# Kernel optimization log

Measured on AMD Instinct MI355X. Metric: run time of the kernel, lower is better.

The kernel has to match this reference:

```python
import jax, jax.numpy as jnp
import numpy as np

H, W = 8, 8
N = 1 + H * W          # 65 tokens (cls + patches)
DIM = 128
HEADS = 8
DH = 32
INNER = HEADS * DH     # 256
B = 64
EPS = 1e-5


def setup_inputs() -> dict:
    key = jax.random.key(0)
    ks = jax.random.split(key, 7)
    x = jax.random.normal(ks[0], (B, N, DIM), dtype=jnp.float32)
    gamma = jnp.ones((DIM,), jnp.float32)
    beta = jnp.zeros((DIM,), jnp.float32)
    # kaiming_uniform-ish init scale for linear weights
    s_qk = float(np.sqrt(1.0 / DIM))
    Wqk = jax.random.uniform(ks[1], (DIM, 2 * INNER), jnp.float32, -s_qk, s_qk)
    # per-(query, key)-position value weights: [n, n, dim, inner]
    Wv = jax.random.uniform(ks[2], (N, N, DIM, INNER), jnp.float32, -s_qk, s_qk)
    s_o = float(np.sqrt(1.0 / INNER))
    Wout = jax.random.uniform(ks[3], (INNER, DIM), jnp.float32, -s_o, s_o)
    bout = jax.random.uniform(ks[4], (DIM,), jnp.float32, -s_o, s_o)
    return {"x": x, "gamma": gamma, "beta": beta, "Wqk": Wqk, "Wv": Wv,
            "Wout": Wout, "bout": bout}


def reference(x, gamma, beta, Wqk, Wv, Wout, bout):
    b, n, d = x.shape
    # LayerNorm
    mu = jnp.mean(x, axis=-1, keepdims=True)
    var = jnp.mean(jnp.square(x - mu), axis=-1, keepdims=True)
    xn = (x - mu) / jnp.sqrt(var + EPS) * gamma + beta
    # q, k projections
    qk = xn @ Wqk                               # [b, n, 2*inner]
    q, k = jnp.split(qk, 2, axis=-1)
    q = q.reshape(b, n, HEADS, DH).transpose(0, 2, 1, 3)  # [b, h, n, dh]
    k = k.reshape(b, n, HEADS, DH).transpose(0, 2, 1, 3)
    scale = DH ** -0.5
    dots = jnp.einsum('bhnd,bhmd->bhnm', q, k) * scale
    attn = jax.nn.softmax(dots, axis=-1)        # [b, h, n, m]
    # per-(n,m) value: v[b,n,m] = xn[b,n] @ Wv[n,m]  -> [b, n, m, inner]
    v = jnp.einsum('bnd,nmde->bnme', xn, Wv)
    v = v.reshape(b, n, n, HEADS, DH)           # [b, n, m, h, dh]
    # weighted sum over keys m
    out = jnp.einsum('bhnm,bnmhd->bnhd', attn, v).reshape(b, n, INNER)
    return out @ Wout + bout
```

## Files before the change

### kernel.cpp

```cpp
#include <hip/hip_runtime.h>

#define EPS 1e-5f

typedef __attribute__((ext_vector_type(8))) short short8;
typedef __attribute__((ext_vector_type(4))) float float4v;

__device__ __forceinline__ unsigned short f2bf(float x) {
  unsigned int u = __builtin_bit_cast(unsigned int, x);
  u += 0x7fffu + ((u >> 16) & 1u);
  return (unsigned short)(u >> 16);
}
__device__ __forceinline__ float bf2f(unsigned short h) {
  unsigned int u = ((unsigned int)h) << 16;
  return __builtin_bit_cast(float, u);
}

__global__ __launch_bounds__(256) void ln_kernel(
    const float* __restrict__ x, const float* __restrict__ gamma,
    const float* __restrict__ beta, float* __restrict__ xn) {
  const int row = blockIdx.x * 4 + (threadIdx.x >> 6);
  const int lane = threadIdx.x & 63;
  const float2 v = ((const float2*)(x + (size_t)row * 128))[lane];
  float s = v.x + v.y;
#pragma unroll
  for (int off = 1; off < 64; off <<= 1) s += __shfl_xor(s, off);
  const float mu = s * (1.f / 128.f);
  const float dx = v.x - mu, dy = v.y - mu;
  float qv = dx * dx + dy * dy;
#pragma unroll
  for (int off = 1; off < 64; off <<= 1) qv += __shfl_xor(qv, off);
  const float rstd = 1.f / sqrtf(qv * (1.f / 128.f) + EPS);
  const float2 g = ((const float2*)gamma)[lane];
  const float2 be = ((const float2*)beta)[lane];
  float2 o;
  o.x = dx * rstd * g.x + be.x;
  o.y = dy * rstd * g.y + be.y;
  ((float2*)(xn + (size_t)row * 128))[lane] = o;
}

__global__ __launch_bounds__(256) void qk_kernel(
    const float* __restrict__ xn, const float* __restrict__ Wqk,
    float* __restrict__ qk) {
  __shared__ float xsx[32][130];
  __shared__ float wsx[128][68];
  const int t = threadIdx.x;
  const int r0 = blockIdx.x * 32, c0 = blockIdx.y * 64;
  for (int i = t; i < 32 * 32; i += 256) {
    int r = i >> 5, c = (i & 31) << 2;
    float4 v = *(const float4*)(xn + (size_t)(r0 + r) * 128 + c);
    float* dst = &xsx[r][c];
    dst[0] = v.x; dst[1] = v.y; dst[2] = v.z; dst[3] = v.w;
  }
  for (int i = t; i < 128 * 16; i += 256) {
    int k = i >> 4, c = (i & 15) << 2;
    *(float4*)&wsx[k][c] = *(const float4*)(Wqk + (size_t)k * 512 + c0 + c);
  }
  __syncthreads();
  const int rr = (t >> 4) * 2, cc = (t & 15) * 4;
  float acc[2][4] = {{0.f, 0.f, 0.f, 0.f}, {0.f, 0.f, 0.f, 0.f}};
  for (int k = 0; k < 128; k++) {
    float4 wv4 = *(const float4*)&wsx[k][cc];
    float x0 = xsx[rr][k], x1 = xsx[rr + 1][k];
    acc[0][0] += x0 * wv4.x; acc[0][1] += x0 * wv4.y;
    acc[0][2] += x0 * wv4.z; acc[0][3] += x0 * wv4.w;
    acc[1][0] += x1 * wv4.x; acc[1][1] += x1 * wv4.y;
    acc[1][2] += x1 * wv4.z; acc[1][3] += x1 * wv4.w;
  }
#pragma unroll
  for (int r = 0; r < 2; r++) {
    float4 o;
    o.x = acc[r][0]; o.y = acc[r][1]; o.z = acc[r][2]; o.w = acc[r][3];
    *(float4*)(qk + (size_t)(r0 + rr + r) * 512 + c0 + cc) = o;
  }
}

__global__ __launch_bounds__(256) void softmax_kernel(
    const float* __restrict__ qk, float* __restrict__ attnT) {
  const int b = blockIdx.x >> 3, h = blockIdx.x & 7;
  __shared__ float qs[65][33];
  __shared__ float ks[65][33];
  __shared__ float dotsS[65][66];
  __shared__ float rsum[65];
  const int t = threadIdx.x;
  for (int i = t; i < 65 * 32; i += 256) {
    int n = i >> 5, d = i & 31;
    size_t base = ((size_t)b * 65 + n) * 512 + h * 32 + d;
    qs[n][d] = qk[base];
    ks[n][d] = qk[base + 256];
  }
  __syncthreads();
  const float scale = 0.17677669529663687f;
  for (int i = t; i < 65 * 65; i += 256) {
    int n = i / 65, mm = i - n * 65;
    float s = 0.f;
#pragma unroll
    for (int d = 0; d < 32; d++) s += qs[n][d] * ks[mm][d];
    dotsS[n][mm] = s * scale;
  }
  __syncthreads();
  if (t < 65) {
    float mx = -1e30f;
    for (int mm = 0; mm < 65; mm++) mx = fmaxf(mx, dotsS[t][mm]);
    float sum = 0.f;
    for (int mm = 0; mm < 65; mm++) {
      float e = __expf(dotsS[t][mm] - mx);
      dotsS[t][mm] = e;
      sum += e;
    }
    rsum[t] = 1.f / sum;
  }
  __syncthreads();
  for (int i = t; i < 65 * 65; i += 256) {
    int n = i / 65, mm = i - n * 65;
    attnT[(((size_t)h * 65 + n) * 65 + mm) * 64 + b] = dotsS[n][mm] * rsum[n];
  }
}

__global__ __launch_bounds__(256, 4) void attnv_kernel(
    const float* __restrict__ xn, const float* __restrict__ attnT,
    const float* __restrict__ Wv, float* __restrict__ innerp) {
  __shared__ __align__(16) unsigned short wvb[2][4096];
  __shared__ float attnL[33 * 64];

  const int nq = blockIdx.x >> 4;
  const int h = (blockIdx.x >> 1) & 7;
  const int half = blockIdx.x & 1;
  const int m0 = half * 33;
  const int mlen = half ? 32 : 33;

  const int t = threadIdx.x, lane = t & 63, w = t >> 6;
  const int boff = w * 16;
  const int er = lane & 15, q = lane >> 4;

  const int e = t & 31;
  const int d0 = (t >> 5) * 16;
  const int kc0 = d0 >> 3;
  const float* wbase = Wv + ((size_t)nq * 65 + m0) * 32768 + (size_t)h * 32 + e;

  float stg[16];
  {
    const float* p = wbase + (size_t)d0 * 256;
#pragma unroll
    for (int i = 0; i < 16; i++) stg[i] = p[(size_t)i * 256];
  }

  {
    const float* abase = attnT + (((size_t)h * 65 + nq) * 65 + m0) * 64;
    for (int i = t; i < mlen * 64; i += 256) attnL[i] = abase[i];
  }

  short8 ah[4], al[4];
  {
    const float* arow = xn + ((size_t)(boff + er) * 65 + nq) * 128;
#pragma unroll
    for (int s = 0; s < 4; s++) {
      float4 v0 = *(const float4*)(arow + s * 32 + q * 8);
      float4 v1 = *(const float4*)(arow + s * 32 + q * 8 + 4);
      float xv[8] = {v0.x, v0.y, v0.z, v0.w, v1.x, v1.y, v1.z, v1.w};
#pragma unroll
      for (int j = 0; j < 8; j++) {
        unsigned short hi = f2bf(xv[j]);
        ah[s][j] = (short)hi;
        al[s][j] = (short)f2bf(xv[j] - bf2f(hi));
      }
    }
  }

  {
    short8 w0, w1;
#pragma unroll
    for (int j = 0; j < 8; j++) {
      w0[j] = (short)f2bf(stg[j]);
      w1[j] = (short)f2bf(stg[8 + j]);
    }
    *(short8*)&wvb[0][e * 128 + ((kc0 ^ (e & 15)) << 3)] = w0;
    *(short8*)&wvb[0][e * 128 + (((kc0 + 1) ^ (e & 15)) << 3)] = w1;
  }
  __syncthreads();

  float4v acc0 = {0.f, 0.f, 0.f, 0.f}, acc1 = {0.f, 0.f, 0.f, 0.f};

  for (int m = 0; m < mlen; m++) {
    const int cur = m & 1;
    if (m + 1 < mlen) {
      const float* p = wbase + (size_t)(m + 1) * 32768 + (size_t)d0 * 256;
#pragma unroll
      for (int i = 0; i < 16; i++) stg[i] = p[(size_t)i * 256];
    }
    const unsigned short* wb = wvb[cur];
    float4v P0 = {0.f, 0.f, 0.f, 0.f}, P1 = {0.f, 0.f, 0.f, 0.f};
#pragma unroll
    for (int s = 0; s < 4; s++) {
      const int kc = 4 * s + q;
      short8 b0 = *(const short8*)&wb[er * 128 + ((kc ^ er) << 3)];
      short8 b1 = *(const short8*)&wb[(er + 16) * 128 + ((kc ^ er) << 3)];
      P0 = __builtin_amdgcn_mfma_f32_16x16x32_bf16(ah[s], b0, P0, 0, 0, 0);
      P1 = __builtin_amdgcn_mfma_f32_16x16x32_bf16(ah[s], b1, P1, 0, 0, 0);
      P0 = __builtin_amdgcn_mfma_f32_16x16x32_bf16(al[s], b0, P0, 0, 0, 0);
      P1 = __builtin_amdgcn_mfma_f32_16x16x32_bf16(al[s], b1, P1, 0, 0, 0);
    }
    {
      const float* ap = attnL + m * 64 + boff + q * 4;
#pragma unroll
      for (int r = 0; r < 4; r++) {
        float av = ap[r];
        acc0[r] += av * P0[r];
        acc1[r] += av * P1[r];
      }
    }
    if (m + 1 < mlen) {
      short8 w0, w1;
#pragma unroll
      for (int j = 0; j < 8; j++) {
        w0[j] = (short)f2bf(stg[j]);
        w1[j] = (short)f2bf(stg[8 + j]);
      }
      unsigned short* wbw = wvb[1 - cur];
      *(short8*)&wbw[e * 128 + ((kc0 ^ (e & 15)) << 3)] = w0;
      *(short8*)&wbw[e * 128 + (((kc0 + 1) ^ (e & 15)) << 3)] = w1;
    }
    __syncthreads();
  }

  float* ip = innerp + (size_t)half * 1064960;
#pragma unroll
  for (int r = 0; r < 4; r++) {
    int b = boff + q * 4 + r;
    size_t o = ((size_t)b * 65 + nq) * 256 + h * 32;
    ip[o + er] = acc0[r];
    ip[o + 16 + er] = acc1[r];
  }
}

__global__ __launch_bounds__(256) void outproj_kernel(
    const float* __restrict__ inner0, const float* __restrict__ inner1,
    const float* __restrict__ Wout, const float* __restrict__ bout,
    float* __restrict__ out) {
  __shared__ float isx[16][258];
  __shared__ float wsx[64][132];
  const int t = threadIdx.x;
  const int r0 = blockIdx.x * 16;
  for (int i = t; i < 16 * 64; i += 256) {
    int r = i >> 6, c = (i & 63) << 2;
    size_t off = (size_t)(r0 + r) * 256 + c;
    float4 v0 = *(const float4*)(inner0 + off);
    float4 v1 = *(const float4*)(inner1 + off);
    float* dst = &isx[r][c];
    dst[0] = v0.x + v1.x; dst[1] = v0.y + v1.y;
    dst[2] = v0.z + v1.z; dst[3] = v0.w + v1.w;
  }
  const int rr = (t >> 5) * 2, cc = (t & 31) * 4;
  float acc[2][4] = {{0.f, 0.f, 0.f, 0.f}, {0.f, 0.f, 0.f, 0.f}};
  for (int kc = 0; kc < 4; kc++) {
    __syncthreads();
    for (int i = t; i < 64 * 32; i += 256) {
      int k = i >> 5, c = (i & 31) << 2;
      *(float4*)&wsx[k][c] = *(const float4*)(Wout + (size_t)(kc * 64 + k) * 128 + c);
    }
    __syncthreads();
#pragma unroll 8
    for (int k = 0; k < 64; k++) {
      float4 wv4 = *(const float4*)&wsx[k][cc];
      float x0 = isx[rr][kc * 64 + k];
      float x1 = isx[rr + 1][kc * 64 + k];
      acc[0][0] += x0 * wv4.x; acc[0][1] += x0 * wv4.y;
      acc[0][2] += x0 * wv4.z; acc[0][3] += x0 * wv4.w;
      acc[1][0] += x1 * wv4.x; acc[1][1] += x1 * wv4.y;
      acc[1][2] += x1 * wv4.z; acc[1][3] += x1 * wv4.w;
    }
  }
  float4 bb = *(const float4*)(bout + cc);
#pragma unroll
  for (int r = 0; r < 2; r++) {
    float4 o;
    o.x = acc[r][0] + bb.x; o.y = acc[r][1] + bb.y;
    o.z = acc[r][2] + bb.z; o.w = acc[r][3] + bb.w;
    *(float4*)(out + (size_t)(r0 + rr + r) * 128 + cc) = o;
  }
}

extern "C" void kernel_launch(void* const* d_in, const int* in_sizes, int n_in,
                              void* d_out, int out_size, void* d_ws, size_t ws_size,
                              hipStream_t stream) {
  const float* x     = (const float*)d_in[0];
  const float* gamma = (const float*)d_in[1];
  const float* beta  = (const float*)d_in[2];
  const float* Wqk   = (const float*)d_in[3];
  const float* Wv    = (const float*)d_in[4];
  const float* Wout  = (const float*)d_in[5];
  const float* bout  = (const float*)d_in[6];
  float* out = (float*)d_out;
  float* ws  = (float*)d_ws;

  float* xn    = ws;
  float* qk    = ws + 532480;
  float* attnT = ws + 2662400;
  float* inner = ws + 4825600;

  ln_kernel<<<1040, 256, 0, stream>>>(x, gamma, beta, xn);
  qk_kernel<<<dim3(130, 8), 256, 0, stream>>>(xn, Wqk, qk);
  softmax_kernel<<<512, 256, 0, stream>>>(qk, attnT);
  attnv_kernel<<<1040, 256, 0, stream>>>(xn, attnT, Wv, inner);
  outproj_kernel<<<260, 256, 0, stream>>>(inner, inner + 1064960, Wout, bout, out);
}
```

Before: 809.3 us.

## Retile attn-V kernel across all heads per block and drop split-bf16 precision

The attn-V kernel now has each 512-thread block cover all 256 inner columns (every head) for one query position and a quarter of the key range, in place of one head and half the keys. Wv tiles of 64x256 move through a larger double-buffered LDS buffer. The xn operand no longer uses the hi/lo bf16 split, which halves the MFMA count but lowers accuracy to a single bf16 rounding. Partial sums are written to four slices that the output projection now adds together, which costs extra workspace traffic.

```diff
diff --git a/kernel.cpp b/kernel.cpp
--- a/kernel.cpp
+++ b/kernel.cpp
@@ -9,10 +9,6 @@
   unsigned int u = __builtin_bit_cast(unsigned int, x);
   u += 0x7fffu + ((u >> 16) & 1u);
   return (unsigned short)(u >> 16);
-}
-__device__ __forceinline__ float bf2f(unsigned short h) {
-  unsigned int u = ((unsigned int)h) << 16;
-  return __builtin_bit_cast(float, u);
 }
 
 __global__ __launch_bounds__(256) void ln_kernel(
@@ -116,126 +112,125 @@
   }
 }
 
-__global__ __launch_bounds__(256, 4) void attnv_kernel(
+__global__ __launch_bounds__(512, 4) void attnv_kernel(
     const float* __restrict__ xn, const float* __restrict__ attnT,
     const float* __restrict__ Wv, float* __restrict__ innerp) {
-  __shared__ __align__(16) unsigned short wvb[2][4096];
-  __shared__ float attnL[33 * 64];
-
-  const int nq = blockIdx.x >> 4;
-  const int h = (blockIdx.x >> 1) & 7;
-  const int half = blockIdx.x & 1;
-  const int m0 = half * 33;
-  const int mlen = half ? 32 : 33;
-
-  const int t = threadIdx.x, lane = t & 63, w = t >> 6;
-  const int boff = w * 16;
+  __shared__ __align__(16) unsigned short buf[2][16384];
+
+  const int nq = blockIdx.x >> 2;
+  const int c = blockIdx.x & 3;
+  const int m0 = c ? (c * 16 + 1) : 0;
+  const int mlen = c ? 16 : 17;
+
+  const int t = threadIdx.x;
+  const int w = t >> 6, lane = t & 63;
+  const int e_col = (w & 3) * 64 + lane;
+  const int dg = w >> 2;
+  const int bt = w >> 1, eh = w & 1;
   const int er = lane & 15, q = lane >> 4;
 
-  const int e = t & 31;
-  const int d0 = (t >> 5) * 16;
-  const int kc0 = d0 >> 3;
-  const float* wbase = Wv + ((size_t)nq * 65 + m0) * 32768 + (size_t)h * 32 + e;
-
-  float stg[16];
+  const float* wtile = Wv + ((size_t)nq * 65 + m0) * 32768 + (size_t)dg * 8192 + e_col;
+
+  float stg[32];
+#pragma unroll
+  for (int i = 0; i < 32; i++) stg[i] = wtile[(size_t)i * 256];
+
+  short8 afr[4];
   {
-    const float* p = wbase + (size_t)d0 * 256;
-#pragma unroll
-    for (int i = 0; i < 16; i++) stg[i] = p[(size_t)i * 256];
-  }
-
-  {
-    const float* abase = attnT + (((size_t)h * 65 + nq) * 65 + m0) * 64;
-    for (int i = t; i < mlen * 64; i += 256) attnL[i] = abase[i];
-  }
-
-  short8 ah[4], al[4];
-  {
-    const float* arow = xn + ((size_t)(boff + er) * 65 + nq) * 128;
-#pragma unroll
-    for (int s = 0; s < 4; s++) {
-      float4 v0 = *(const float4*)(arow + s * 32 + q * 8);
-      float4 v1 = *(const float4*)(arow + s * 32 + q * 8 + 4);
-      float xv[8] = {v0.x, v0.y, v0.z, v0.w, v1.x, v1.y, v1.z, v1.w};
-#pragma unroll
-      for (int j = 0; j < 8; j++) {
-        unsigned short hi = f2bf(xv[j]);
-        ah[s][j] = (short)hi;
-        al[s][j] = (short)f2bf(xv[j] - bf2f(hi));
+    const float* arow = xn + ((size_t)(bt * 16 + er) * 65 + nq) * 128;
+#pragma unroll
+    for (int idx = 0; idx < 4; idx++) {
+      float4 v0 = *(const float4*)(arow + idx * 32 + q * 8);
+      float4 v1 = *(const float4*)(arow + idx * 32 + q * 8 + 4);
+      short8 a;
+      a[0] = (short)f2bf(v0.x); a[1] = (short)f2bf(v0.y);
+      a[2] = (short)f2bf(v0.z); a[3] = (short)f2bf(v0.w);
+      a[4] = (short)f2bf(v1.x); a[5] = (short)f2bf(v1.y);
+      a[6] = (short)f2bf(v1.z); a[7] = (short)f2bf(v1.w);
+      afr[idx] = a;
+    }
+  }
+
+  float4 av4[4];
+#define LOAD_AV(m)                                                            \
+  {                                                                           \
+    _Pragma("unroll")                                                         \
+    for (int hg = 0; hg < 4; hg++) {                                          \
+      size_t off = ((size_t)((eh * 4 + hg) * 65 + nq) * 65 + (m)) * 64 +      \
+                   bt * 16 + q * 4;                                           \
+      av4[hg] = *(const float4*)(attnT + off);                                \
+    }                                                                         \
+  }
+  LOAD_AV(m0);
+
+#define WRITE_BUF(bsel)                                                       \
+  {                                                                           \
+    unsigned short* dst = buf[bsel] + e_col * 64;                             \
+    _Pragma("unroll")                                                         \
+    for (int cj = 0; cj < 4; cj++) {                                          \
+      int ch = dg * 4 + cj;                                                   \
+      int slot = ch ^ (e_col & 7);                                            \
+      short8 pk;                                                              \
+      _Pragma("unroll")                                                       \
+      for (int j = 0; j < 8; j++) pk[j] = (short)f2bf(stg[cj * 8 + j]);       \
+      *(short8*)(dst + slot * 8) = pk;                                        \
+    }                                                                         \
+  }
+  WRITE_BUF(0);
+#pragma unroll
+  for (int i = 0; i < 32; i++) stg[i] = wtile[16384 + (size_t)i * 256];
+  __syncthreads();
+
+  float4v acc[8];
+#pragma unroll
+  for (int el = 0; el < 8; el++) acc[el] = (float4v){0.f, 0.f, 0.f, 0.f};
+
+  const int S = 2 * mlen;
+  for (int step = 0; step < S; step++) {
+    const int cur = step & 1;
+    const unsigned short* bb = buf[cur];
+    const short8 a0 = afr[(step & 1) * 2], a1 = afr[(step & 1) * 2 + 1];
+#pragma unroll
+    for (int el = 0; el < 8; el++) {
+      const unsigned short* rp = bb + ((eh * 8 + el) * 16 + er) * 64;
+      float4v P = {0.f, 0.f, 0.f, 0.f};
+      short8 B0 = *(const short8*)(rp + ((q ^ (er & 7)) << 3));
+      short8 B1 = *(const short8*)(rp + (((4 + q) ^ (er & 7)) << 3));
+      P = __builtin_amdgcn_mfma_f32_16x16x32_bf16(a0, B0, P, 0, 0, 0);
+      P = __builtin_amdgcn_mfma_f32_16x16x32_bf16(a1, B1, P, 0, 0, 0);
+      const float4 av = av4[el >> 1];
+      acc[el][0] += av.x * P[0];
+      acc[el][1] += av.y * P[1];
+      acc[el][2] += av.z * P[2];
+      acc[el][3] += av.w * P[3];
+    }
+    if (step + 1 < S) {
+      WRITE_BUF(1 - cur);
+      if (step + 2 < S) {
+        const int ns = step + 2;
+        const float* p = wtile + (size_t)(ns >> 1) * 32768 + (size_t)(ns & 1) * 16384;
+#pragma unroll
+        for (int i = 0; i < 32; i++) stg[i] = p[(size_t)i * 256];
       }
-    }
-  }
-
-  {
-    short8 w0, w1;
-#pragma unroll
-    for (int j = 0; j < 8; j++) {
-      w0[j] = (short)f2bf(stg[j]);
-      w1[j] = (short)f2bf(stg[8 + j]);
-    }
-    *(short8*)&wvb[0][e * 128 + ((kc0 ^ (e & 15)) << 3)] = w0;
-    *(short8*)&wvb[0][e * 128 + (((kc0 + 1) ^ (e & 15)) << 3)] = w1;
-  }
-  __syncthreads();
-
-  float4v acc0 = {0.f, 0.f, 0.f, 0.f}, acc1 = {0.f, 0.f, 0.f, 0.f};
-
-  for (int m = 0; m < mlen; m++) {
-    const int cur = m & 1;
-    if (m + 1 < mlen) {
-      const float* p = wbase + (size_t)(m + 1) * 32768 + (size_t)d0 * 256;
-#pragma unroll
-      for (int i = 0; i < 16; i++) stg[i] = p[(size_t)i * 256];
-    }
-    const unsigned short* wb = wvb[cur];
-    float4v P0 = {0.f, 0.f, 0.f, 0.f}, P1 = {0.f, 0.f, 0.f, 0.f};
-#pragma unroll
-    for (int s = 0; s < 4; s++) {
-      const int kc = 4 * s + q;
-      short8 b0 = *(const short8*)&wb[er * 128 + ((kc ^ er) << 3)];
-      short8 b1 = *(const short8*)&wb[(er + 16) * 128 + ((kc ^ er) << 3)];
-      P0 = __builtin_amdgcn_mfma_f32_16x16x32_bf16(ah[s], b0, P0, 0, 0, 0);
-      P1 = __builtin_amdgcn_mfma_f32_16x16x32_bf16(ah[s], b1, P1, 0, 0, 0);
-      P0 = __builtin_amdgcn_mfma_f32_16x16x32_bf16(al[s], b0, P0, 0, 0, 0);
-      P1 = __builtin_amdgcn_mfma_f32_16x16x32_bf16(al[s], b1, P1, 0, 0, 0);
-    }
-    {
-      const float* ap = attnL + m * 64 + boff + q * 4;
-#pragma unroll
-      for (int r = 0; r < 4; r++) {
-        float av = ap[r];
-        acc0[r] += av * P0[r];
-        acc1[r] += av * P1[r];
-      }
-    }
-    if (m + 1 < mlen) {
-      short8 w0, w1;
-#pragma unroll
-      for (int j = 0; j < 8; j++) {
-        w0[j] = (short)f2bf(stg[j]);
-        w1[j] = (short)f2bf(stg[8 + j]);
-      }
-      unsigned short* wbw = wvb[1 - cur];
-      *(short8*)&wbw[e * 128 + ((kc0 ^ (e & 15)) << 3)] = w0;
-      *(short8*)&wbw[e * 128 + (((kc0 + 1) ^ (e & 15)) << 3)] = w1;
+      if ((step & 1) == 1) LOAD_AV(m0 + (step >> 1) + 1);
     }
     __syncthreads();
   }
 
-  float* ip = innerp + (size_t)half * 1064960;
-#pragma unroll
-  for (int r = 0; r < 4; r++) {
-    int b = boff + q * 4 + r;
-    size_t o = ((size_t)b * 65 + nq) * 256 + h * 32;
-    ip[o + er] = acc0[r];
-    ip[o + 16 + er] = acc1[r];
+  float* ip = innerp + (size_t)c * 1064960;
+#pragma unroll
+  for (int el = 0; el < 8; el++) {
+#pragma unroll
+    for (int r = 0; r < 4; r++) {
+      int brow = bt * 16 + q * 4 + r;
+      ip[((size_t)brow * 65 + nq) * 256 + (eh * 8 + el) * 16 + er] = acc[el][r];
+    }
   }
 }
 
 __global__ __launch_bounds__(256) void outproj_kernel(
-    const float* __restrict__ inner0, const float* __restrict__ inner1,
-    const float* __restrict__ Wout, const float* __restrict__ bout,
-    float* __restrict__ out) {
+    const float* __restrict__ inner, const float* __restrict__ Wout,
+    const float* __restrict__ bout, float* __restrict__ out) {
   __shared__ float isx[16][258];
   __shared__ float wsx[64][132];
   const int t = threadIdx.x;
@@ -243,11 +238,15 @@
   for (int i = t; i < 16 * 64; i += 256) {
     int r = i >> 6, c = (i & 63) << 2;
     size_t off = (size_t)(r0 + r) * 256 + c;
-    float4 v0 = *(const float4*)(inner0 + off);
-    float4 v1 = *(const float4*)(inner1 + off);
+    float4 v0 = *(const float4*)(inner + off);
+    float4 v1 = *(const float4*)(inner + 1064960 + off);
+    float4 v2 = *(const float4*)(inner + 2129920 + off);
+    float4 v3 = *(const float4*)(inner + 3194880 + off);
     float* dst = &isx[r][c];
-    dst[0] = v0.x + v1.x; dst[1] = v0.y + v1.y;
-    dst[2] = v0.z + v1.z; dst[3] = v0.w + v1.w;
+    dst[0] = v0.x + v1.x + v2.x + v3.x;
+    dst[1] = v0.y + v1.y + v2.y + v3.y;
+    dst[2] = v0.z + v1.z + v2.z + v3.z;
+    dst[3] = v0.w + v1.w + v2.w + v3.w;
   }
   const int rr = (t >> 5) * 2, cc = (t & 31) * 4;
   float acc[2][4] = {{0.f, 0.f, 0.f, 0.f}, {0.f, 0.f, 0.f, 0.f}};
@@ -300,6 +299,6 @@
   ln_kernel<<<1040, 256, 0, stream>>>(x, gamma, beta, xn);
   qk_kernel<<<dim3(130, 8), 256, 0, stream>>>(xn, Wqk, qk);
   softmax_kernel<<<512, 256, 0, stream>>>(qk, attnT);
-  attnv_kernel<<<1040, 256, 0, stream>>>(xn, attnT, Wv, inner);
-  outproj_kernel<<<260, 256, 0, stream>>>(inner, inner + 1064960, Wout, bout, out);
-}
+  attnv_kernel<<<260, 512, 0, stream>>>(xn, attnT, Wv, inner);
+  outproj_kernel<<<260, 256, 0, stream>>>(inner, Wout, bout, out);
+}
```

Result: slower. 917.5 us (+13.4%).
